# Optimization experiments

Hardware: AMD Instinct MI355X
Metric: run time of the kernel (lower is better)

Reference implementation:

```python
import jax, jax.numpy as jnp
import numpy as np

D_MODEL, D_STATE, DT_RANK = 1024, 16, 64
B_SZ, T_LEN = 2, 2048


def setup_inputs() -> dict:
    key = jax.random.key(0)
    k1, k2, k3, k4 = jax.random.split(key, 4)
    x = jax.random.normal(k1, (B_SZ, T_LEN, D_MODEL), dtype=jnp.float32)
    # x_proj: Linear(d_model -> dt_rank + 2*d_state), no bias
    W_xproj = jax.random.normal(k2, (DT_RANK + 2 * D_STATE, D_MODEL), dtype=jnp.float32) / np.sqrt(D_MODEL)
    # dt_proj: Linear(dt_rank -> d_model), std=0.01 weight, uniform(-log(d_state), log(d_state)) bias
    W_dt = 0.01 * jax.random.normal(k3, (D_MODEL, DT_RANK), dtype=jnp.float32)
    b_dt = jax.random.uniform(k4, (D_MODEL,), dtype=jnp.float32,
                              minval=-np.log(D_STATE), maxval=np.log(D_STATE))
    # A_log = log(arange(1..d_state)) per channel
    A_log = jnp.log(jnp.arange(1, D_STATE + 1, dtype=jnp.float32))[None, :].repeat(D_MODEL, axis=0)
    Dp = jnp.ones((D_MODEL,), dtype=jnp.float32)
    return {"x": x, "W_xproj": W_xproj, "W_dt": W_dt, "b_dt": b_dt, "A_log": A_log, "Dp": Dp}


def reference(x, W_xproj, W_dt, b_dt, A_log, Dp):
    dt_rank = W_dt.shape[1]
    d_s = A_log.shape[1]
    xz = jnp.einsum('btd,pd->btp', x, W_xproj)              # (B,T,dt_rank+2*ds)
    dt_raw = xz[..., :dt_rank]
    Bm = xz[..., dt_rank:dt_rank + d_s]                     # (B,T,ds)
    Cm = xz[..., dt_rank + d_s:]                            # (B,T,ds)
    dt = jax.nn.softplus(jnp.einsum('btr,dr->btd', dt_raw, W_dt) + b_dt)  # (B,T,d)
    A = -jnp.exp(A_log)                                     # (d,ds)
    dA = jnp.exp(dt[..., None] * A)                         # (B,T,d,ds)
    dBx = dt[..., None] * Bm[:, :, None, :] * x[..., None]  # (B,T,d,ds): dB * x

    def step(h, inp):
        dA_t, dBx_t, C_t = inp                               # (B,d,ds),(B,d,ds),(B,ds)
        h = dA_t * h + dBx_t
        y = jnp.einsum('bds,bs->bd', h, C_t)
        return h, y

    h0 = jnp.zeros((x.shape[0], x.shape[2], d_s), dtype=x.dtype)
    _, ys = jax.lax.scan(step, h0, (dA.transpose(1, 0, 2, 3),
                                    dBx.transpose(1, 0, 2, 3),
                                    Cm.transpose(1, 0, 2)))   # ys: (T,B,d)
    out = ys.transpose(1, 0, 2)
    return out + Dp * x
```

## Files before the change

### kernel.cpp

```cpp
#include <hip/hip_runtime.h>
#include <hip/hip_bf16.h>

#define BB 2
#define TT 2048
#define DD 1024
#define SS 16
#define RR 64
#define PP 96
#define BT (BB*TT)
#define NC 128
#define CL 16
#define KS 4

#define OFF_XZ   0
#define OFF_DT   1572864
#define OFF_PH   3670016
#define OFF_PH2  8126464
#define OFF_BC   12320768

__global__ __launch_bounds__(256, 4) void k_proj1(const float* __restrict__ x,
                                                  const float* __restrict__ Wx,
                                                  float* __restrict__ xzp) {
    __shared__ float wlds[96 * 68];
    const int blk  = blockIdx.x;
    const int tile = blk & 255;
    const int ks   = blk >> 8;
    const int rt0  = tile * 16;
    const int k0   = ks * 256;
    const int tid  = threadIdx.x;
    const int tg   = tid >> 5;
    const int pg   = tid & 31;

    float acc[2][3] = {};
    const float* xbase = x + (size_t)rt0 * DD;

    #pragma unroll
    for (int kt = 0; kt < 4; ++kt) {
        const int kk0 = k0 + kt * 64;
        #pragma unroll
        for (int j = 0; j < 6; ++j) {
            int f4 = tid + 256 * j;
            int p  = f4 >> 4;
            int c4 = f4 & 15;
            float4 v = *(const float4*)(Wx + (size_t)p * DD + kk0 + c4 * 4);
            *(float4*)(&wlds[p * 68 + c4 * 4]) = v;
        }
        __syncthreads();
        #pragma unroll 4
        for (int k4 = 0; k4 < 16; ++k4) {
            float4 xv[2];
            #pragma unroll
            for (int i = 0; i < 2; ++i)
                xv[i] = *(const float4*)(xbase + (size_t)(tg * 2 + i) * DD + kk0 + k4 * 4);
            #pragma unroll
            for (int j = 0; j < 3; ++j) {
                float4 wv = *(const float4*)(&wlds[(pg * 3 + j) * 68 + k4 * 4]);
                #pragma unroll
                for (int i = 0; i < 2; ++i)
                    acc[i][j] += xv[i].x * wv.x + xv[i].y * wv.y
                               + xv[i].z * wv.z + xv[i].w * wv.w;
            }
        }
        __syncthreads();
    }
    float* outp = xzp + (size_t)ks * (BT * PP);
    #pragma unroll
    for (int i = 0; i < 2; ++i)
        #pragma unroll
        for (int j = 0; j < 3; ++j)
            outp[(size_t)(rt0 + tg * 2 + i) * PP + pg * 3 + j] = acc[i][j];
}

__global__ __launch_bounds__(256, 4) void k_proj2(const float* __restrict__ xzp,
                                                  const float* __restrict__ Wdt,
                                                  const float* __restrict__ bdt,
                                                  __hip_bfloat16* __restrict__ dtb,
                                                  float* __restrict__ bc) {
    __shared__ float xzs[16 * 64];
    const int blk   = blockIdx.x;
    const int ttile = blk & 255;
    const int dtile = blk >> 8;
    const int rt0   = ttile * 16;
    const int tid   = threadIdx.x;
    const int d     = dtile * 256 + tid;

    {
        int row = tid >> 4;
        int c4  = tid & 15;
        float4 s = make_float4(0.f, 0.f, 0.f, 0.f);
        #pragma unroll
        for (int slot = 0; slot < KS; ++slot) {
            float4 v = *(const float4*)(xzp + (size_t)slot * (BT * PP)
                                        + (size_t)(rt0 + row) * PP + c4 * 4);
            s.x += v.x; s.y += v.y; s.z += v.z; s.w += v.w;
        }
        *(float4*)(&xzs[row * 64 + c4 * 4]) = s;
    }
    if (dtile == 0 && tid < 128) {
        int row = tid >> 3;
        int c4  = tid & 7;
        float4 s = make_float4(0.f, 0.f, 0.f, 0.f);
        #pragma unroll
        for (int slot = 0; slot < KS; ++slot) {
            float4 v = *(const float4*)(xzp + (size_t)slot * (BT * PP)
                                        + (size_t)(rt0 + row) * PP + 64 + c4 * 4);
            s.x += v.x; s.y += v.y; s.z += v.z; s.w += v.w;
        }
        *(float4*)(bc + (size_t)(rt0 + row) * 32 + c4 * 4) = s;
    }
    __syncthreads();

    const float* wrow = Wdt + (size_t)d * RR;
    float4 w0  = *(const float4*)(wrow +  0), w1  = *(const float4*)(wrow +  4);
    float4 w2  = *(const float4*)(wrow +  8), w3  = *(const float4*)(wrow + 12);
    float4 w4  = *(const float4*)(wrow + 16), w5  = *(const float4*)(wrow + 20);
    float4 w6  = *(const float4*)(wrow + 24), w7  = *(const float4*)(wrow + 28);
    float4 w8  = *(const float4*)(wrow + 32), w9  = *(const float4*)(wrow + 36);
    float4 w10 = *(const float4*)(wrow + 40), w11 = *(const float4*)(wrow + 44);
    float4 w12 = *(const float4*)(wrow + 48), w13 = *(const float4*)(wrow + 52);
    float4 w14 = *(const float4*)(wrow + 56), w15 = *(const float4*)(wrow + 60);
    const float bv = bdt[d];

#define P2STEP(acc, r4, wv) { float4 a = *(const float4*)(&xzs[t * 64 + (r4) * 4]); \
        acc += a.x * wv.x + a.y * wv.y + a.z * wv.z + a.w * wv.w; }

    #pragma unroll 2
    for (int t = 0; t < 16; ++t) {
        float a0 = bv, a1 = 0.f, a2 = 0.f, a3 = 0.f;
        P2STEP(a0, 0, w0)   P2STEP(a1, 1, w1)   P2STEP(a2, 2, w2)   P2STEP(a3, 3, w3)
        P2STEP(a0, 4, w4)   P2STEP(a1, 5, w5)   P2STEP(a2, 6, w6)   P2STEP(a3, 7, w7)
        P2STEP(a0, 8, w8)   P2STEP(a1, 9, w9)   P2STEP(a2, 10, w10) P2STEP(a3, 11, w11)
        P2STEP(a0, 12, w12) P2STEP(a1, 13, w13) P2STEP(a2, 14, w14) P2STEP(a3, 15, w15)
        float acc = (a0 + a1) + (a2 + a3);
        float sp = (acc > 20.f) ? acc : log1pf(expf(acc));
        dtb[(size_t)(rt0 + t) * DD + d] = __float2bfloat16(sp);
    }
#undef P2STEP
}

#define POWER_TREE(e1, ep) \
    const float e2_ = (e1) * (e1), e4_ = e2_ * e2_, e8_ = e4_ * e4_; \
    ep[0] = (e1);        ep[1] = e2_;         ep[2] = e2_ * (e1);  ep[3] = e4_; \
    ep[4] = e4_ * (e1);  ep[5] = e4_ * e2_;   ep[6] = ep[5] * (e1); ep[7] = e8_; \
    ep[8] = e8_ * (e1);  ep[9] = e8_ * e2_;   ep[10] = ep[9] * (e1); ep[11] = e8_ * e4_; \
    ep[12] = ep[11] * (e1); ep[13] = ep[11] * e2_; ep[14] = ep[13] * (e1); ep[15] = e8_ * e8_;

__global__ __launch_bounds__(256, 4) void k_pass1(const __hip_bfloat16* __restrict__ dtb,
                                                  const float* __restrict__ x,
                                                  const float* __restrict__ bc,
                                                  const float* __restrict__ Alog,
                                                  float* __restrict__ ph) {
    const int blk   = blockIdx.x;
    const int dtile = blk & 3;
    const int c     = (blk >> 2) & 127;
    const int b     = blk >> 9;
    const int tid   = threadIdx.x;
    const int d     = dtile * 256 + tid;

    const float an0 = -expf(Alog[(size_t)d * SS]) * 1.44269504f;

    float h[16];
    #pragma unroll
    for (int s = 0; s < 16; ++s) h[s] = 0.f;
    float sdt = 0.f;

    const int t0 = c * CL;
    #pragma unroll 2
    for (int t = 0; t < CL; ++t) {
        const size_t rt = (size_t)b * TT + t0 + t;
        const float dtv = __bfloat162float(dtb[rt * DD + d]);
        const float xv  = x[rt * DD + d];
        const float u   = dtv * xv;
        const float e1  = exp2f(dtv * an0);
        sdt += dtv;
        const float* bcrow = bc + rt * 32;
        float ep[16];
        POWER_TREE(e1, ep)
        #pragma unroll
        for (int s4 = 0; s4 < 4; ++s4) {
            float4 bm = *(const float4*)(bcrow + s4 * 4);
            float bmv[4] = {bm.x, bm.y, bm.z, bm.w};
            #pragma unroll
            for (int q = 0; q < 4; ++q) {
                const int s = s4 * 4 + q;
                h[s] = ep[s] * h[s] + u * bmv[q];
            }
        }
    }

    float* base = ph + ((size_t)(b * NC + c) * 17) * DD + d;
    base[0] = sdt;
    #pragma unroll
    for (int s = 0; s < 16; ++s)
        base[(size_t)(1 + s) * DD] = h[s];
}

__global__ __launch_bounds__(128) void k_pass2(const float* __restrict__ Alog,
                                               const float* __restrict__ ph,
                                               float* __restrict__ ph2) {
    const int gid = blockIdx.x * 128 + threadIdx.x;
    const int d = gid & 1023;
    const int s = (gid >> 10) & 15;
    const int b = gid >> 14;
    const float anse = -expf(Alog[(size_t)d * SS]) * 1.44269504f * (float)(s + 1);

    const size_t sdt_base = ((size_t)b * NC) * 17 * DD + d;
    const size_t h_base   = sdt_base + (size_t)(1 + s) * DD;
    const size_t o_base   = ((size_t)b * NC) * 16 * DD + (size_t)s * DD + d;

    float h = 0.f;
    for (int cg = 0; cg < NC; cg += 8) {
        float sdt_[8], hh_[8];
        #pragma unroll
        for (int k = 0; k < 8; ++k) {
            const size_t coff = (size_t)(cg + k) * (17 * DD);
            sdt_[k] = ph[sdt_base + coff];
            hh_[k]  = ph[h_base + coff];
        }
        #pragma unroll
        for (int k = 0; k < 8; ++k) {
            ph2[o_base + (size_t)(cg + k) * (16 * DD)] = h;
            h = hh_[k] + exp2f(anse * sdt_[k]) * h;
        }
    }
}

__global__ __launch_bounds__(256, 4) void k_pass3(const __hip_bfloat16* __restrict__ dtb,
                                                  const float* __restrict__ x,
                                                  const float* __restrict__ bc,
                                                  const float* __restrict__ Alog,
                                                  const float* __restrict__ ph2,
                                                  const float* __restrict__ Dp,
                                                  float* __restrict__ out) {
    const int blk   = blockIdx.x;
    const int dtile = blk & 3;
    const int c     = (blk >> 2) & 127;
    const int b     = blk >> 9;
    const int tid   = threadIdx.x;
    const int d     = dtile * 256 + tid;

    const float an0 = -expf(Alog[(size_t)d * SS]) * 1.44269504f;

    float h[16];
    const float* base = ph2 + ((size_t)(b * NC + c) * 16) * DD + d;
    #pragma unroll
    for (int s = 0; s < 16; ++s)
        h[s] = base[(size_t)s * DD];

    const float dpv = Dp[d];
    const int t0 = c * CL;
    #pragma unroll 2
    for (int t = 0; t < CL; ++t) {
        const size_t rt = (size_t)b * TT + t0 + t;
        const float dtv = __bfloat162float(dtb[rt * DD + d]);
        const float xv  = x[rt * DD + d];
        const float u   = dtv * xv;
        const float e1  = exp2f(dtv * an0);
        const float* bcrow = bc + rt * 32;
        float ep[16];
        POWER_TREE(e1, ep)
        float yp[4] = {0.f, 0.f, 0.f, 0.f};
        #pragma unroll
        for (int s4 = 0; s4 < 4; ++s4) {
            float4 bm = *(const float4*)(bcrow + s4 * 4);
            float4 cm = *(const float4*)(bcrow + 16 + s4 * 4);
            float bmv[4] = {bm.x, bm.y, bm.z, bm.w};
            float cmv[4] = {cm.x, cm.y, cm.z, cm.w};
            #pragma unroll
            for (int q = 0; q < 4; ++q) {
                const int s = s4 * 4 + q;
                h[s] = ep[s] * h[s] + u * bmv[q];
                yp[s4] += h[s] * cmv[q];
            }
        }
        out[rt * DD + d] = (yp[0] + yp[1]) + (yp[2] + yp[3]) + dpv * xv;
    }
}

extern "C" void kernel_launch(void* const* d_in, const int* in_sizes, int n_in,
                              void* d_out, int out_size, void* d_ws, size_t ws_size,
                              hipStream_t stream) {
    const float* x    = (const float*)d_in[0];
    const float* Wx   = (const float*)d_in[1];
    const float* Wdt  = (const float*)d_in[2];
    const float* bdt  = (const float*)d_in[3];
    const float* Alog = (const float*)d_in[4];
    const float* Dp   = (const float*)d_in[5];
    float* out = (float*)d_out;
    float* ws  = (float*)d_ws;

    float* xzp = ws + OFF_XZ;
    __hip_bfloat16* dtb = (__hip_bfloat16*)(ws + OFF_DT);
    float* ph  = ws + OFF_PH;
    float* ph2 = ws + OFF_PH2;
    float* bc  = ws + OFF_BC;

    k_proj1<<<1024, 256, 0, stream>>>(x, Wx, xzp);
    k_proj2<<<1024, 256, 0, stream>>>(xzp, Wdt, bdt, dtb, bc);
    k_pass1<<<1024, 256, 0, stream>>>(dtb, x, bc, Alog, ph);
    k_pass2<<<256, 128, 0, stream>>>(Alog, ph, ph2);
    k_pass3<<<1024, 256, 0, stream>>>(dtb, x, bc, Alog, ph2, Dp, out);
}
```

Baseline: 171.6 us.

## Fuse five kernels into one persistent kernel with atomic grid barriers

Replaces the five separate launches with a single persistent kernel of 512 blocks. Each block processes two work units per phase, and phases are separated by atomic-counter grid barriers, with a memset beforehand to reset the counters. The aim is to remove per-launch overhead and the inter-kernel drain gaps. In exchange it adds spin-wait barrier cost, concentrates the serial pass2 scan on only 128 blocks while the rest idle, and depends on all 512 blocks being co-resident to avoid deadlock.

```diff
diff --git a/kernel.cpp b/kernel.cpp
--- a/kernel.cpp
+++ b/kernel.cpp
@@ -11,23 +11,41 @@
 #define NC 128
 #define CL 16
 #define KS 4
+#define NB 512
 
 #define OFF_XZ   0
 #define OFF_DT   1572864
 #define OFF_PH   3670016
 #define OFF_PH2  8126464
 #define OFF_BC   12320768
-
-__global__ __launch_bounds__(256, 4) void k_proj1(const float* __restrict__ x,
-                                                  const float* __restrict__ Wx,
-                                                  float* __restrict__ xzp) {
-    __shared__ float wlds[96 * 68];
-    const int blk  = blockIdx.x;
-    const int tile = blk & 255;
-    const int ks   = blk >> 8;
+#define OFF_BAR  12451840
+
+__device__ __forceinline__ void gridbar(int* bar, int idx) {
+    __syncthreads();
+    if (threadIdx.x == 0) {
+        __hip_atomic_fetch_add(&bar[idx], 1, __ATOMIC_ACQ_REL, __HIP_MEMORY_SCOPE_AGENT);
+        while (__hip_atomic_load(&bar[idx], __ATOMIC_ACQUIRE, __HIP_MEMORY_SCOPE_AGENT) < NB)
+            __builtin_amdgcn_s_sleep(2);
+    }
+    __syncthreads();
+}
+
+#define POWER_TREE(e1, ep) \
+    const float e2_ = (e1) * (e1), e4_ = e2_ * e2_, e8_ = e4_ * e4_; \
+    ep[0] = (e1);        ep[1] = e2_;         ep[2] = e2_ * (e1);  ep[3] = e4_; \
+    ep[4] = e4_ * (e1);  ep[5] = e4_ * e2_;   ep[6] = ep[5] * (e1); ep[7] = e8_; \
+    ep[8] = e8_ * (e1);  ep[9] = e8_ * e2_;   ep[10] = ep[9] * (e1); ep[11] = e8_ * e4_; \
+    ep[12] = ep[11] * (e1); ep[13] = ep[11] * e2_; ep[14] = ep[13] * (e1); ep[15] = e8_ * e8_;
+
+__device__ __forceinline__ void phaseA(int u, int tid,
+                                       const float* __restrict__ x,
+                                       const float* __restrict__ Wx,
+                                       float* __restrict__ xzp,
+                                       float* __restrict__ wlds) {
+    const int tile = u & 255;
+    const int ks   = u >> 8;
     const int rt0  = tile * 16;
     const int k0   = ks * 256;
-    const int tid  = threadIdx.x;
     const int tg   = tid >> 5;
     const int pg   = tid & 31;
 
@@ -71,19 +89,19 @@
             outp[(size_t)(rt0 + tg * 2 + i) * PP + pg * 3 + j] = acc[i][j];
 }
 
-__global__ __launch_bounds__(256, 4) void k_proj2(const float* __restrict__ xzp,
-                                                  const float* __restrict__ Wdt,
-                                                  const float* __restrict__ bdt,
-                                                  __hip_bfloat16* __restrict__ dtb,
-                                                  float* __restrict__ bc) {
-    __shared__ float xzs[16 * 64];
-    const int blk   = blockIdx.x;
-    const int ttile = blk & 255;
-    const int dtile = blk >> 8;
+__device__ __forceinline__ void phaseB(int u, int tid,
+                                       const float* __restrict__ xzp,
+                                       const float* __restrict__ Wdt,
+                                       const float* __restrict__ bdt,
+                                       __hip_bfloat16* __restrict__ dtb,
+                                       float* __restrict__ bc,
+                                       float* __restrict__ xzs) {
+    const int ttile = u & 255;
+    const int dtile = u >> 8;
     const int rt0   = ttile * 16;
-    const int tid   = threadIdx.x;
     const int d     = dtile * 256 + tid;
 
+    __syncthreads();
     {
         int row = tid >> 4;
         int c4  = tid & 15;
@@ -138,23 +156,15 @@
 #undef P2STEP
 }
 
-#define POWER_TREE(e1, ep) \
-    const float e2_ = (e1) * (e1), e4_ = e2_ * e2_, e8_ = e4_ * e4_; \
-    ep[0] = (e1);        ep[1] = e2_;         ep[2] = e2_ * (e1);  ep[3] = e4_; \
-    ep[4] = e4_ * (e1);  ep[5] = e4_ * e2_;   ep[6] = ep[5] * (e1); ep[7] = e8_; \
-    ep[8] = e8_ * (e1);  ep[9] = e8_ * e2_;   ep[10] = ep[9] * (e1); ep[11] = e8_ * e4_; \
-    ep[12] = ep[11] * (e1); ep[13] = ep[11] * e2_; ep[14] = ep[13] * (e1); ep[15] = e8_ * e8_;
-
-__global__ __launch_bounds__(256, 4) void k_pass1(const __hip_bfloat16* __restrict__ dtb,
-                                                  const float* __restrict__ x,
-                                                  const float* __restrict__ bc,
-                                                  const float* __restrict__ Alog,
-                                                  float* __restrict__ ph) {
-    const int blk   = blockIdx.x;
-    const int dtile = blk & 3;
-    const int c     = (blk >> 2) & 127;
-    const int b     = blk >> 9;
-    const int tid   = threadIdx.x;
+__device__ __forceinline__ void phaseC(int u, int tid,
+                                       const __hip_bfloat16* __restrict__ dtb,
+                                       const float* __restrict__ x,
+                                       const float* __restrict__ bc,
+                                       const float* __restrict__ Alog,
+                                       float* __restrict__ ph) {
+    const int dtile = u & 3;
+    const int c     = (u >> 2) & 127;
+    const int b     = u >> 9;
     const int d     = dtile * 256 + tid;
 
     const float an0 = -expf(Alog[(size_t)d * SS]) * 1.44269504f;
@@ -170,7 +180,7 @@
         const size_t rt = (size_t)b * TT + t0 + t;
         const float dtv = __bfloat162float(dtb[rt * DD + d]);
         const float xv  = x[rt * DD + d];
-        const float u   = dtv * xv;
+        const float u_  = dtv * xv;
         const float e1  = exp2f(dtv * an0);
         sdt += dtv;
         const float* bcrow = bc + rt * 32;
@@ -183,7 +193,7 @@
             #pragma unroll
             for (int q = 0; q < 4; ++q) {
                 const int s = s4 * 4 + q;
-                h[s] = ep[s] * h[s] + u * bmv[q];
+                h[s] = ep[s] * h[s] + u_ * bmv[q];
             }
         }
     }
@@ -195,10 +205,10 @@
         base[(size_t)(1 + s) * DD] = h[s];
 }
 
-__global__ __launch_bounds__(128) void k_pass2(const float* __restrict__ Alog,
-                                               const float* __restrict__ ph,
-                                               float* __restrict__ ph2) {
-    const int gid = blockIdx.x * 128 + threadIdx.x;
+__device__ __forceinline__ void phaseD(int gid,
+                                       const float* __restrict__ Alog,
+                                       const float* __restrict__ ph,
+                                       float* __restrict__ ph2) {
     const int d = gid & 1023;
     const int s = (gid >> 10) & 15;
     const int b = gid >> 14;
@@ -225,18 +235,17 @@
     }
 }
 
-__global__ __launch_bounds__(256, 4) void k_pass3(const __hip_bfloat16* __restrict__ dtb,
-                                                  const float* __restrict__ x,
-                                                  const float* __restrict__ bc,
-                                                  const float* __restrict__ Alog,
-                                                  const float* __restrict__ ph2,
-                                                  const float* __restrict__ Dp,
-                                                  float* __restrict__ out) {
-    const int blk   = blockIdx.x;
-    const int dtile = blk & 3;
-    const int c     = (blk >> 2) & 127;
-    const int b     = blk >> 9;
-    const int tid   = threadIdx.x;
+__device__ __forceinline__ void phaseE(int u, int tid,
+                                       const __hip_bfloat16* __restrict__ dtb,
+                                       const float* __restrict__ x,
+                                       const float* __restrict__ bc,
+                                       const float* __restrict__ Alog,
+                                       const float* __restrict__ ph2,
+                                       const float* __restrict__ Dp,
+                                       float* __restrict__ out) {
+    const int dtile = u & 3;
+    const int c     = (u >> 2) & 127;
+    const int b     = u >> 9;
     const int d     = dtile * 256 + tid;
 
     const float an0 = -expf(Alog[(size_t)d * SS]) * 1.44269504f;
@@ -254,7 +263,7 @@
         const size_t rt = (size_t)b * TT + t0 + t;
         const float dtv = __bfloat162float(dtb[rt * DD + d]);
         const float xv  = x[rt * DD + d];
-        const float u   = dtv * xv;
+        const float u_  = dtv * xv;
         const float e1  = exp2f(dtv * an0);
         const float* bcrow = bc + rt * 32;
         float ep[16];
@@ -269,12 +278,48 @@
             #pragma unroll
             for (int q = 0; q < 4; ++q) {
                 const int s = s4 * 4 + q;
-                h[s] = ep[s] * h[s] + u * bmv[q];
+                h[s] = ep[s] * h[s] + u_ * bmv[q];
                 yp[s4] += h[s] * cmv[q];
             }
         }
         out[rt * DD + d] = (yp[0] + yp[1]) + (yp[2] + yp[3]) + dpv * xv;
     }
+}
+
+__global__ __launch_bounds__(256, 4) void k_fused(const float* __restrict__ x,
+                                                  const float* __restrict__ Wx,
+                                                  const float* __restrict__ Wdt,
+                                                  const float* __restrict__ bdt,
+                                                  const float* __restrict__ Alog,
+                                                  const float* __restrict__ Dp,
+                                                  float* __restrict__ out,
+                                                  float* __restrict__ xzp,
+                                                  __hip_bfloat16* __restrict__ dtb,
+                                                  float* __restrict__ ph,
+                                                  float* __restrict__ ph2,
+                                                  float* __restrict__ bc,
+                                                  int* __restrict__ bar) {
+    __shared__ float smem[96 * 68];
+    const int bid = blockIdx.x;
+    const int tid = threadIdx.x;
+
+    phaseA(bid,       tid, x, Wx, xzp, smem);
+    phaseA(bid + 512, tid, x, Wx, xzp, smem);
+    gridbar(bar, 0);
+
+    phaseB(bid,       tid, xzp, Wdt, bdt, dtb, bc, smem);
+    phaseB(bid + 512, tid, xzp, Wdt, bdt, dtb, bc, smem);
+    gridbar(bar, 1);
+
+    phaseC(bid,       tid, dtb, x, bc, Alog, ph);
+    phaseC(bid + 512, tid, dtb, x, bc, Alog, ph);
+    gridbar(bar, 2);
+
+    if (bid < 128) phaseD(bid * 256 + tid, Alog, ph, ph2);
+    gridbar(bar, 3);
+
+    phaseE(bid,       tid, dtb, x, bc, Alog, ph2, Dp, out);
+    phaseE(bid + 512, tid, dtb, x, bc, Alog, ph2, Dp, out);
 }
 
 extern "C" void kernel_launch(void* const* d_in, const int* in_sizes, int n_in,
@@ -294,10 +339,9 @@
     float* ph  = ws + OFF_PH;
     float* ph2 = ws + OFF_PH2;
     float* bc  = ws + OFF_BC;
-
-    k_proj1<<<1024, 256, 0, stream>>>(x, Wx, xzp);
-    k_proj2<<<1024, 256, 0, stream>>>(xzp, Wdt, bdt, dtb, bc);
-    k_pass1<<<1024, 256, 0, stream>>>(dtb, x, bc, Alog, ph);
-    k_pass2<<<256, 128, 0, stream>>>(Alog, ph, ph2);
-    k_pass3<<<1024, 256, 0, stream>>>(dtb, x, bc, Alog, ph2, Dp, out);
-}
+    int*   bar = (int*)(ws + OFF_BAR);
+
+    hipMemsetAsync(bar, 0, 4 * sizeof(int), stream);
+    k_fused<<<NB, 256, 0, stream>>>(x, Wx, Wdt, bdt, Alog, Dp, out,
+                                    xzp, dtb, ph, ph2, bc, bar);
+}
```

Result: slower. 436.5 us (+154.4%).

## Fuse dt projection into chunk scan pass and retile x_proj GEMM

Applied to the files above, without the earlier changes.

Merges the dt projection/softplus kernel into the first chunk-scan pass. Each block now computes dt for its own 16-step chunk from the reduced xz rows and uses it directly, instead of writing dt and reading it back. A separate small kernel now reduces the split-K partials of xz in place, and the B/C values are read straight from xz rather than from a separate bc buffer. The x_proj GEMM is retiled to 32 rows per block with a wider LDS pad. The cost is higher register pressure in the fused kernel, whose launch bounds drop to 3 waves, and redundant reads of the xz rows by the four d-tile blocks.

```diff
diff --git a/kernel.cpp b/kernel.cpp
--- a/kernel.cpp
+++ b/kernel.cpp
@@ -12,26 +12,25 @@
 #define CL 16
 #define KS 4
 
-#define OFF_XZ   0
-#define OFF_DT   1572864
-#define OFF_PH   3670016
+#define OFF_XZP  0
+#define OFF_DTB  1572864
+#define OFF_AGG  3670016
 #define OFF_PH2  8126464
-#define OFF_BC   12320768
 
 __global__ __launch_bounds__(256, 4) void k_proj1(const float* __restrict__ x,
                                                   const float* __restrict__ Wx,
                                                   float* __restrict__ xzp) {
-    __shared__ float wlds[96 * 68];
+    __shared__ float wlds[96 * 72];
     const int blk  = blockIdx.x;
-    const int tile = blk & 255;
-    const int ks   = blk >> 8;
-    const int rt0  = tile * 16;
+    const int tile = blk & 127;
+    const int ks   = blk >> 7;
+    const int rt0  = tile * 32;
     const int k0   = ks * 256;
     const int tid  = threadIdx.x;
     const int tg   = tid >> 5;
     const int pg   = tid & 31;
 
-    float acc[2][3] = {};
+    float acc[4][3] = {};
     const float* xbase = x + (size_t)rt0 * DD;
 
     #pragma unroll
@@ -43,20 +42,20 @@
             int p  = f4 >> 4;
             int c4 = f4 & 15;
             float4 v = *(const float4*)(Wx + (size_t)p * DD + kk0 + c4 * 4);
-            *(float4*)(&wlds[p * 68 + c4 * 4]) = v;
+            *(float4*)(&wlds[p * 72 + c4 * 4]) = v;
         }
         __syncthreads();
         #pragma unroll 4
         for (int k4 = 0; k4 < 16; ++k4) {
-            float4 xv[2];
-            #pragma unroll
-            for (int i = 0; i < 2; ++i)
-                xv[i] = *(const float4*)(xbase + (size_t)(tg * 2 + i) * DD + kk0 + k4 * 4);
+            float4 xv[4];
+            #pragma unroll
+            for (int i = 0; i < 4; ++i)
+                xv[i] = *(const float4*)(xbase + (size_t)(tg * 4 + i) * DD + kk0 + k4 * 4);
             #pragma unroll
             for (int j = 0; j < 3; ++j) {
-                float4 wv = *(const float4*)(&wlds[(pg * 3 + j) * 68 + k4 * 4]);
+                float4 wv = *(const float4*)(&wlds[(pg * 3 + j) * 72 + k4 * 4]);
                 #pragma unroll
-                for (int i = 0; i < 2; ++i)
+                for (int i = 0; i < 4; ++i)
                     acc[i][j] += xv[i].x * wv.x + xv[i].y * wv.y
                                + xv[i].z * wv.z + xv[i].w * wv.w;
             }
@@ -65,50 +64,47 @@
     }
     float* outp = xzp + (size_t)ks * (BT * PP);
     #pragma unroll
-    for (int i = 0; i < 2; ++i)
+    for (int i = 0; i < 4; ++i)
         #pragma unroll
         for (int j = 0; j < 3; ++j)
-            outp[(size_t)(rt0 + tg * 2 + i) * PP + pg * 3 + j] = acc[i][j];
-}
-
-__global__ __launch_bounds__(256, 4) void k_proj2(const float* __restrict__ xzp,
+            outp[(size_t)(rt0 + tg * 4 + i) * PP + pg * 3 + j] = acc[i][j];
+}
+
+__global__ __launch_bounds__(256) void k_xzred(float* __restrict__ xzp) {
+    const int i4 = blockIdx.x * 256 + threadIdx.x;
+    float4 a = *(const float4*)(xzp + (size_t)i4 * 4);
+    #pragma unroll
+    for (int slot = 1; slot < KS; ++slot) {
+        float4 v = *(const float4*)(xzp + (size_t)slot * (BT * PP) + (size_t)i4 * 4);
+        a.x += v.x; a.y += v.y; a.z += v.z; a.w += v.w;
+    }
+    *(float4*)(xzp + (size_t)i4 * 4) = a;
+}
+
+#define POWER_TREE(e1, ep) \
+    const float e2_ = (e1) * (e1), e4_ = e2_ * e2_, e8_ = e4_ * e4_; \
+    ep[0] = (e1);        ep[1] = e2_;         ep[2] = e2_ * (e1);  ep[3] = e4_; \
+    ep[4] = e4_ * (e1);  ep[5] = e4_ * e2_;   ep[6] = ep[5] * (e1); ep[7] = e8_; \
+    ep[8] = e8_ * (e1);  ep[9] = e8_ * e2_;   ep[10] = ep[9] * (e1); ep[11] = e8_ * e4_; \
+    ep[12] = ep[11] * (e1); ep[13] = ep[11] * e2_; ep[14] = ep[13] * (e1); ep[15] = e8_ * e8_;
+
+__global__ __launch_bounds__(256, 3) void k_mega1(const float* __restrict__ x,
+                                                  const float* __restrict__ xz,
                                                   const float* __restrict__ Wdt,
                                                   const float* __restrict__ bdt,
+                                                  const float* __restrict__ Alog,
                                                   __hip_bfloat16* __restrict__ dtb,
-                                                  float* __restrict__ bc) {
-    __shared__ float xzs[16 * 64];
+                                                  float* __restrict__ agg) {
     const int blk   = blockIdx.x;
-    const int ttile = blk & 255;
-    const int dtile = blk >> 8;
-    const int rt0   = ttile * 16;
+    const int dtile = blk & 3;
+    const int c     = (blk >> 2) & 127;
+    const int b     = blk >> 9;
     const int tid   = threadIdx.x;
     const int d     = dtile * 256 + tid;
-
-    {
-        int row = tid >> 4;
-        int c4  = tid & 15;
-        float4 s = make_float4(0.f, 0.f, 0.f, 0.f);
-        #pragma unroll
-        for (int slot = 0; slot < KS; ++slot) {
-            float4 v = *(const float4*)(xzp + (size_t)slot * (BT * PP)
-                                        + (size_t)(rt0 + row) * PP + c4 * 4);
-            s.x += v.x; s.y += v.y; s.z += v.z; s.w += v.w;
-        }
-        *(float4*)(&xzs[row * 64 + c4 * 4]) = s;
-    }
-    if (dtile == 0 && tid < 128) {
-        int row = tid >> 3;
-        int c4  = tid & 7;
-        float4 s = make_float4(0.f, 0.f, 0.f, 0.f);
-        #pragma unroll
-        for (int slot = 0; slot < KS; ++slot) {
-            float4 v = *(const float4*)(xzp + (size_t)slot * (BT * PP)
-                                        + (size_t)(rt0 + row) * PP + 64 + c4 * 4);
-            s.x += v.x; s.y += v.y; s.z += v.z; s.w += v.w;
-        }
-        *(float4*)(bc + (size_t)(rt0 + row) * 32 + c4 * 4) = s;
-    }
-    __syncthreads();
+    const int rt0   = b * TT + c * CL;
+
+    const float an0 = -expf(Alog[(size_t)d * SS]) * 1.44269504f;
+    const float bv  = bdt[d];
 
     const float* wrow = Wdt + (size_t)d * RR;
     float4 w0  = *(const float4*)(wrow +  0), w1  = *(const float4*)(wrow +  4);
@@ -119,76 +115,52 @@
     float4 w10 = *(const float4*)(wrow + 40), w11 = *(const float4*)(wrow + 44);
     float4 w12 = *(const float4*)(wrow + 48), w13 = *(const float4*)(wrow + 52);
     float4 w14 = *(const float4*)(wrow + 56), w15 = *(const float4*)(wrow + 60);
-    const float bv = bdt[d];
-
-#define P2STEP(acc, r4, wv) { float4 a = *(const float4*)(&xzs[t * 64 + (r4) * 4]); \
-        acc += a.x * wv.x + a.y * wv.y + a.z * wv.z + a.w * wv.w; }
-
-    #pragma unroll 2
-    for (int t = 0; t < 16; ++t) {
+
+    float e1v[CL], u[CL], sdt = 0.f;
+
+#define GSTEP(acc, r4, wv) { float4 a_ = *(const float4*)(xrow + (r4) * 4); \
+        acc += a_.x * wv.x + a_.y * wv.y + a_.z * wv.z + a_.w * wv.w; }
+
+    #pragma unroll
+    for (int t = 0; t < CL; ++t) {
+        const float* xrow = xz + (size_t)(rt0 + t) * PP;
         float a0 = bv, a1 = 0.f, a2 = 0.f, a3 = 0.f;
-        P2STEP(a0, 0, w0)   P2STEP(a1, 1, w1)   P2STEP(a2, 2, w2)   P2STEP(a3, 3, w3)
-        P2STEP(a0, 4, w4)   P2STEP(a1, 5, w5)   P2STEP(a2, 6, w6)   P2STEP(a3, 7, w7)
-        P2STEP(a0, 8, w8)   P2STEP(a1, 9, w9)   P2STEP(a2, 10, w10) P2STEP(a3, 11, w11)
-        P2STEP(a0, 12, w12) P2STEP(a1, 13, w13) P2STEP(a2, 14, w14) P2STEP(a3, 15, w15)
+        GSTEP(a0, 0, w0)   GSTEP(a1, 1, w1)   GSTEP(a2, 2, w2)   GSTEP(a3, 3, w3)
+        GSTEP(a0, 4, w4)   GSTEP(a1, 5, w5)   GSTEP(a2, 6, w6)   GSTEP(a3, 7, w7)
+        GSTEP(a0, 8, w8)   GSTEP(a1, 9, w9)   GSTEP(a2, 10, w10) GSTEP(a3, 11, w11)
+        GSTEP(a0, 12, w12) GSTEP(a1, 13, w13) GSTEP(a2, 14, w14) GSTEP(a3, 15, w15)
         float acc = (a0 + a1) + (a2 + a3);
-        float sp = (acc > 20.f) ? acc : log1pf(expf(acc));
-        dtb[(size_t)(rt0 + t) * DD + d] = __float2bfloat16(sp);
-    }
-#undef P2STEP
-}
-
-#define POWER_TREE(e1, ep) \
-    const float e2_ = (e1) * (e1), e4_ = e2_ * e2_, e8_ = e4_ * e4_; \
-    ep[0] = (e1);        ep[1] = e2_;         ep[2] = e2_ * (e1);  ep[3] = e4_; \
-    ep[4] = e4_ * (e1);  ep[5] = e4_ * e2_;   ep[6] = ep[5] * (e1); ep[7] = e8_; \
-    ep[8] = e8_ * (e1);  ep[9] = e8_ * e2_;   ep[10] = ep[9] * (e1); ep[11] = e8_ * e4_; \
-    ep[12] = ep[11] * (e1); ep[13] = ep[11] * e2_; ep[14] = ep[13] * (e1); ep[15] = e8_ * e8_;
-
-__global__ __launch_bounds__(256, 4) void k_pass1(const __hip_bfloat16* __restrict__ dtb,
-                                                  const float* __restrict__ x,
-                                                  const float* __restrict__ bc,
-                                                  const float* __restrict__ Alog,
-                                                  float* __restrict__ ph) {
-    const int blk   = blockIdx.x;
-    const int dtile = blk & 3;
-    const int c     = (blk >> 2) & 127;
-    const int b     = blk >> 9;
-    const int tid   = threadIdx.x;
-    const int d     = dtile * 256 + tid;
-
-    const float an0 = -expf(Alog[(size_t)d * SS]) * 1.44269504f;
+        const float dt = (acc > 20.f) ? acc : log1pf(expf(acc));
+        dtb[(size_t)(rt0 + t) * DD + d] = __float2bfloat16(dt);
+        const float xv = x[(size_t)(rt0 + t) * DD + d];
+        u[t]   = dt * xv;
+        e1v[t] = exp2f(dt * an0);
+        sdt   += dt;
+    }
+#undef GSTEP
 
     float h[16];
     #pragma unroll
     for (int s = 0; s < 16; ++s) h[s] = 0.f;
-    float sdt = 0.f;
-
-    const int t0 = c * CL;
-    #pragma unroll 2
+
+    #pragma unroll
     for (int t = 0; t < CL; ++t) {
-        const size_t rt = (size_t)b * TT + t0 + t;
-        const float dtv = __bfloat162float(dtb[rt * DD + d]);
-        const float xv  = x[rt * DD + d];
-        const float u   = dtv * xv;
-        const float e1  = exp2f(dtv * an0);
-        sdt += dtv;
-        const float* bcrow = bc + rt * 32;
+        const float* brow = xz + (size_t)(rt0 + t) * PP + 64;
         float ep[16];
-        POWER_TREE(e1, ep)
+        POWER_TREE(e1v[t], ep)
         #pragma unroll
         for (int s4 = 0; s4 < 4; ++s4) {
-            float4 bm = *(const float4*)(bcrow + s4 * 4);
+            float4 bm = *(const float4*)(brow + s4 * 4);
             float bmv[4] = {bm.x, bm.y, bm.z, bm.w};
             #pragma unroll
             for (int q = 0; q < 4; ++q) {
                 const int s = s4 * 4 + q;
-                h[s] = ep[s] * h[s] + u * bmv[q];
+                h[s] = ep[s] * h[s] + u[t] * bmv[q];
             }
         }
     }
 
-    float* base = ph + ((size_t)(b * NC + c) * 17) * DD + d;
+    float* base = agg + ((size_t)(b * NC + c) * 17) * DD + d;
     base[0] = sdt;
     #pragma unroll
     for (int s = 0; s < 16; ++s)
@@ -196,7 +168,7 @@
 }
 
 __global__ __launch_bounds__(128) void k_pass2(const float* __restrict__ Alog,
-                                               const float* __restrict__ ph,
+                                               const float* __restrict__ agg,
                                                float* __restrict__ ph2) {
     const int gid = blockIdx.x * 128 + threadIdx.x;
     const int d = gid & 1023;
@@ -214,8 +186,8 @@
         #pragma unroll
         for (int k = 0; k < 8; ++k) {
             const size_t coff = (size_t)(cg + k) * (17 * DD);
-            sdt_[k] = ph[sdt_base + coff];
-            hh_[k]  = ph[h_base + coff];
+            sdt_[k] = agg[sdt_base + coff];
+            hh_[k]  = agg[h_base + coff];
         }
         #pragma unroll
         for (int k = 0; k < 8; ++k) {
@@ -225,9 +197,9 @@
     }
 }
 
-__global__ __launch_bounds__(256, 4) void k_pass3(const __hip_bfloat16* __restrict__ dtb,
+__global__ __launch_bounds__(256, 4) void k_mega3(const __hip_bfloat16* __restrict__ dtb,
                                                   const float* __restrict__ x,
-                                                  const float* __restrict__ bc,
+                                                  const float* __restrict__ xz,
                                                   const float* __restrict__ Alog,
                                                   const float* __restrict__ ph2,
                                                   const float* __restrict__ Dp,
@@ -238,8 +210,10 @@
     const int b     = blk >> 9;
     const int tid   = threadIdx.x;
     const int d     = dtile * 256 + tid;
+    const int rt0   = b * TT + c * CL;
 
     const float an0 = -expf(Alog[(size_t)d * SS]) * 1.44269504f;
+    const float dpv = Dp[d];
 
     float h[16];
     const float* base = ph2 + ((size_t)(b * NC + c) * 16) * DD + d;
@@ -247,23 +221,20 @@
     for (int s = 0; s < 16; ++s)
         h[s] = base[(size_t)s * DD];
 
-    const float dpv = Dp[d];
-    const int t0 = c * CL;
-    #pragma unroll 2
+    #pragma unroll
     for (int t = 0; t < CL; ++t) {
-        const size_t rt = (size_t)b * TT + t0 + t;
-        const float dtv = __bfloat162float(dtb[rt * DD + d]);
-        const float xv  = x[rt * DD + d];
-        const float u   = dtv * xv;
-        const float e1  = exp2f(dtv * an0);
-        const float* bcrow = bc + rt * 32;
+        const float dt = __bfloat162float(dtb[(size_t)(rt0 + t) * DD + d]);
+        const float xv = x[(size_t)(rt0 + t) * DD + d];
+        const float u  = dt * xv;
+        const float e1 = exp2f(dt * an0);
+        const float* brow = xz + (size_t)(rt0 + t) * PP + 64;
         float ep[16];
         POWER_TREE(e1, ep)
         float yp[4] = {0.f, 0.f, 0.f, 0.f};
         #pragma unroll
         for (int s4 = 0; s4 < 4; ++s4) {
-            float4 bm = *(const float4*)(bcrow + s4 * 4);
-            float4 cm = *(const float4*)(bcrow + 16 + s4 * 4);
+            float4 bm = *(const float4*)(brow + s4 * 4);
+            float4 cm = *(const float4*)(brow + 16 + s4 * 4);
             float bmv[4] = {bm.x, bm.y, bm.z, bm.w};
             float cmv[4] = {cm.x, cm.y, cm.z, cm.w};
             #pragma unroll
@@ -273,7 +244,7 @@
                 yp[s4] += h[s] * cmv[q];
             }
         }
-        out[rt * DD + d] = (yp[0] + yp[1]) + (yp[2] + yp[3]) + dpv * xv;
+        out[(size_t)(rt0 + t) * DD + d] = (yp[0] + yp[1]) + (yp[2] + yp[3]) + dpv * xv;
     }
 }
 
@@ -289,15 +260,14 @@
     float* out = (float*)d_out;
     float* ws  = (float*)d_ws;
 
-    float* xzp = ws + OFF_XZ;
-    __hip_bfloat16* dtb = (__hip_bfloat16*)(ws + OFF_DT);
-    float* ph  = ws + OFF_PH;
+    float* xzp = ws + OFF_XZP;
+    __hip_bfloat16* dtb = (__hip_bfloat16*)(ws + OFF_DTB);
+    float* agg = ws + OFF_AGG;
     float* ph2 = ws + OFF_PH2;
-    float* bc  = ws + OFF_BC;
-
-    k_proj1<<<1024, 256, 0, stream>>>(x, Wx, xzp);
-    k_proj2<<<1024, 256, 0, stream>>>(xzp, Wdt, bdt, dtb, bc);
-    k_pass1<<<1024, 256, 0, stream>>>(dtb, x, bc, Alog, ph);
-    k_pass2<<<256, 128, 0, stream>>>(Alog, ph, ph2);
-    k_pass3<<<1024, 256, 0, stream>>>(dtb, x, bc, Alog, ph2, Dp, out);
-}
+
+    k_proj1<<<512, 256, 0, stream>>>(x, Wx, xzp);
+    k_xzred<<<384, 256, 0, stream>>>(xzp);
+    k_mega1<<<1024, 256, 0, stream>>>(x, xzp, Wdt, bdt, Alog, dtb, agg);
+    k_pass2<<<256, 128, 0, stream>>>(Alog, agg, ph2);
+    k_mega3<<<1024, 256, 0, stream>>>(dtb, x, xzp, Alog, ph2, Dp, out);
+}
```

After: 182.1 us. 6.1% more time.
